# Kernel tuning notes

Measured on AMD Instinct MI355X. Metric: run time of the kernel, lower is better.

The kernel has to match this reference:

```python
import jax, jax.numpy as jnp
import numpy as np

B, T, QL, KVL, D, H = 4, 512, 2, 1, 1024, 16
N = T * QL          # query tokens for self-attn
HD = D // H
MLP_H = 4 * D
EPS_ADA = 1e-6
EPS_LN = 1e-5
NEG = -10000.0


def _ln(x, eps):
    mu = jnp.mean(x, axis=-1, keepdims=True)
    xc = x - mu
    var = jnp.mean(xc * xc, axis=-1, keepdims=True)
    return xc * jax.lax.rsqrt(var + eps)


def _attention(xq, xk, xv, wq, wk, wv, wo, bo, mask, pad_add):
    # xq:[B,Nq,D] xk/xv:[B,Nk,D]; mask:[Nq,Nk] bool; pad_add:[B,1,1,Nk]
    qh = (xq @ wq).reshape(B, -1, H, HD).transpose(0, 2, 1, 3)
    kh = (xk @ wk).reshape(B, -1, H, HD).transpose(0, 2, 1, 3)
    vh = (xv @ wv).reshape(B, -1, H, HD).transpose(0, 2, 1, 3)
    dots = jnp.einsum('bhnd,bhmd->bhnm', qh, kh) * (HD ** -0.5)
    dots = jnp.where(mask[None, None], dots, jnp.asarray(NEG, dots.dtype))
    dots = dots + pad_add
    attn = jax.nn.softmax(dots, axis=-1)
    out = jnp.einsum('bhnm,bhmd->bhnd', attn, vh)
    out = out.transpose(0, 2, 1, 3).reshape(B, -1, D)
    return out @ wo + bo


def setup_inputs() -> dict:
    key = jax.random.key(0)
    ks = jax.random.split(key, 32)
    s = 0.02
    d = {
        'q': jax.random.normal(ks[0], (B, N, D), jnp.float32),
        'c': jax.random.normal(ks[1], (B, T, D), jnp.float32),
        'pe': jax.random.normal(ks[2], (B, T, D), jnp.float32),
        'padding_mask': jax.random.randint(ks[3], (B, T), 0, 2, jnp.int32),
        'w_mod': jax.random.normal(ks[4], (D, 6 * D), jnp.float32) * s,
        'b_mod': jnp.zeros((6 * D,), jnp.float32),
        'sa_wq': jax.random.normal(ks[5], (D, D), jnp.float32) * s,
        'sa_wk': jax.random.normal(ks[6], (D, D), jnp.float32) * s,
        'sa_wv': jax.random.normal(ks[7], (D, D), jnp.float32) * s,
        'sa_wo': jax.random.normal(ks[8], (D, D), jnp.float32) * s,
        'sa_bo': jnp.zeros((D,), jnp.float32),
        'ca_wq': jax.random.normal(ks[9], (D, D), jnp.float32) * s,
        'ca_wk': jax.random.normal(ks[10], (D, D), jnp.float32) * s,
        'ca_wv': jax.random.normal(ks[11], (D, D), jnp.float32) * s,
        'ca_wo': jax.random.normal(ks[12], (D, D), jnp.float32) * s,
        'ca_bo': jnp.zeros((D,), jnp.float32),
        'gk': jnp.ones((D,), jnp.float32), 'bk': jnp.zeros((D,), jnp.float32),
        'gv': jnp.ones((D,), jnp.float32), 'bv': jnp.zeros((D,), jnp.float32),
        'w_alpha': jax.random.normal(ks[13], (2 * D, D), jnp.float32) * s,
        'b_alpha': jnp.zeros((D,), jnp.float32),
        'w1': jax.random.normal(ks[14], (D, MLP_H), jnp.float32) * s,
        'b1': jnp.zeros((MLP_H,), jnp.float32),
        'w2': jax.random.normal(ks[15], (MLP_H, D), jnp.float32) * s,
        'b2': jnp.zeros((D,), jnp.float32),
    }
    return d


def reference(q, c, pe, padding_mask, w_mod, b_mod,
              sa_wq, sa_wk, sa_wv, sa_wo, sa_bo,
              ca_wq, ca_wk, ca_wv, ca_wo, ca_bo,
              gk, bk, gv, bv, w_alpha, b_alpha, w1, b1, w2, b2):
    # AdaLN modulation from condition c
    mod = jax.nn.silu(c) @ w_mod + b_mod                    # [B,T,6D]
    scale_sa, shift_sa, scale_ca, shift_ca, scale_mlp, shift_mlp = jnp.split(mod, 6, axis=2)
    rep = lambda t: jnp.repeat(t, QL, axis=1)               # [B,T,D]->[B,N,D]

    # masks
    causal = jnp.tril(jnp.ones((N, N), bool))
    tril_t = jnp.tril(jnp.ones((T, T), bool))
    cross_mask = jnp.repeat(jnp.repeat(tril_t, QL, axis=0), KVL, axis=1)  # [N, T*KVL]
    pad_f = padding_mask.astype(q.dtype)
    pad_sa = (jnp.repeat(pad_f, QL, axis=1) * NEG)[:, None, None, :]      # keys len N
    pad_ca = (jnp.repeat(pad_f, KVL, axis=1) * NEG)[:, None, None, :]     # keys len T

    # self-attention (pre-norm + modulation)
    q1 = _ln(q, EPS_ADA) * (1 + rep(scale_sa)) + rep(shift_sa)
    q1 = _attention(q1, q1, q1, sa_wq, sa_wk, sa_wv, sa_wo, sa_bo, causal, pad_sa)
    q = q1 + q

    # cross-attention with custom mask
    q2 = _ln(q, EPS_ADA) * (1 + rep(scale_ca)) + rep(shift_ca)
    kin = _ln(c + pe, EPS_LN) * gk + bk
    vin = _ln(c, EPS_LN) * gv + bv
    q2 = _attention(q2, kin, vin, ca_wq, ca_wk, ca_wv, ca_wo, ca_bo, cross_mask, pad_ca)
    alpha = jnp.concatenate([q2, q], axis=-1) @ w_alpha + b_alpha
    q = (1 + alpha) * q2 + q

    # MLP
    q3 = _ln(q, EPS_ADA) * (1 + rep(scale_mlp)) + rep(shift_mlp)
    h = jax.nn.gelu(q3 @ w1 + b1, approximate=False)
    q = q + (h @ w2 + b2)
    return q
```

## Files before the change

### kernel.cpp

```cpp
#include <hip/hip_runtime.h>
#include <cstdint>

typedef unsigned short u16;
typedef __attribute__((ext_vector_type(8))) short bf16x8;
typedef __attribute__((ext_vector_type(4))) float f32x4;

#define DEV static __device__ __forceinline__
#define AS1 __attribute__((address_space(1)))
#define AS3 __attribute__((address_space(3)))

static constexpr int Bb = 4, Tt = 512, Nn = 1024, Dd = 1024, Hh = 16;
static constexpr float NEGV = -10000.0f;

DEV u16 f2bf(float f) {
  unsigned int u = __builtin_bit_cast(unsigned int, f);
  u += 0x7fffu + ((u >> 16) & 1u);
  return (u16)(u >> 16);
}
DEV float bf2f(u16 s) {
  unsigned int u = ((unsigned int)s) << 16;
  return __builtin_bit_cast(float, u);
}
DEV f32x4 mfma16(bf16x8 a, bf16x8 b, f32x4 c) {
  return __builtin_amdgcn_mfma_f32_16x16x32_bf16(a, b, c, 0, 0, 0);
}
DEV void gload16(const u16* g, u16* lds) {
  __builtin_amdgcn_global_load_lds((AS1 const unsigned int*)g, (AS3 unsigned int*)lds, 16, 0, 0);
}
DEV int swz8(int wg, int nwg) { const int c = nwg >> 3; return (wg & 7) * c + (wg >> 3); }

__global__ __launch_bounds__(256) void transpose_cast(const float* __restrict__ src,
                                                      u16* __restrict__ dst, int R, int C) {
  __shared__ float tile[32][33];
  const int c0 = blockIdx.x * 32, r0 = blockIdx.y * 32;
  const int tx = threadIdx.x, ty = threadIdx.y;
#pragma unroll
  for (int j = 0; j < 4; ++j)
    tile[ty + 8 * j][tx] = src[(size_t)(r0 + ty + 8 * j) * C + c0 + tx];
  __syncthreads();
#pragma unroll
  for (int j = 0; j < 4; ++j)
    dst[(size_t)(c0 + ty + 8 * j) * R + r0 + tx] = f2bf(tile[tx][ty + 8 * j]);
}

__global__ __launch_bounds__(256) void tr16_k(const u16* __restrict__ src, u16* __restrict__ dst,
                                              int ss, int R) {
  __shared__ u16 tile[32][33];
  const int c0 = blockIdx.x * 32, r0 = blockIdx.y * 32;
  const int tx = threadIdx.x, ty = threadIdx.y;
#pragma unroll
  for (int j = 0; j < 4; ++j)
    tile[ty + 8 * j][tx] = src[(size_t)(r0 + ty + 8 * j) * ss + c0 + tx];
  __syncthreads();
  const int b = r0 / R, rb = r0 - b * R;
#pragma unroll
  for (int j = 0; j < 4; ++j)
    dst[(size_t)b * 1024 * R + (size_t)(c0 + ty + 8 * j) * R + rb + tx] = tile[tx][ty + 8 * j];
}

__global__ __launch_bounds__(256) void silu_k(const float* __restrict__ c, u16* __restrict__ o, int n) {
  int i = blockIdx.x * 256 + threadIdx.x;
  if (i < n) { float x = c[i]; o[i] = f2bf(x / (1.0f + __expf(-x))); }
}

__global__ __launch_bounds__(256) void cat_k(const float* __restrict__ q2, const float* __restrict__ qr,
                                             u16* __restrict__ cat) {
  int i = blockIdx.x * 256 + threadIdx.x;
  int r = i >> 10, c = i & 1023;
  cat[(size_t)r * 2048 + c] = f2bf(q2[i]);
  cat[(size_t)r * 2048 + 1024 + c] = f2bf(qr[i]);
}

__global__ __launch_bounds__(256) void red2_k(const u16* __restrict__ s0, const u16* __restrict__ s1,
                                              const float* __restrict__ bias, const float* __restrict__ res,
                                              float* __restrict__ out) {
  const int i = blockIdx.x * 256 + threadIdx.x;
  const uint2 a = ((const uint2*)s0)[i];
  const uint2 b = ((const uint2*)s1)[i];
  const float4 bv = ((const float4*)bias)[i & 255];
  const float4 rv = ((const float4*)res)[i];
  float4 v;
  v.x = bf2f((u16)(a.x & 0xffff)) + bf2f((u16)(b.x & 0xffff)) + bv.x + rv.x;
  v.y = bf2f((u16)(a.x >> 16))    + bf2f((u16)(b.x >> 16))    + bv.y + rv.y;
  v.z = bf2f((u16)(a.y & 0xffff)) + bf2f((u16)(b.y & 0xffff)) + bv.z + rv.z;
  v.w = bf2f((u16)(a.y >> 16))    + bf2f((u16)(b.y >> 16))    + bv.w + rv.w;
  ((float4*)out)[i] = v;
}

__global__ __launch_bounds__(64) void mrow_k(const int* __restrict__ pm, float* __restrict__ M) {
  const int tid = threadIdx.x;
  const int b = tid >> 4, seg = tid & 15;
  int pre[32];
  int a = 1;
#pragma unroll
  for (int j = 0; j < 32; ++j) { a &= pm[b * 512 + seg * 32 + j]; pre[j] = a; }
  const int total = a;
  int excl = 1;
  for (int s = 0; s < 16; ++s) {
    int o = __shfl(total, (b << 4) + s, 64);
    if (s < seg) excl &= o;
  }
#pragma unroll
  for (int j = 0; j < 32; ++j)
    M[b * 512 + seg * 32 + j] = (excl & pre[j]) ? NEGV : 0.0f;
}

__global__ __launch_bounds__(256) void ln_mod_k(const float* __restrict__ X, const u16* __restrict__ MOD,
                                                u16* __restrict__ OUT, int chunk) {
  const int row = blockIdx.x;
  const int b = row >> 10, i = row & 1023, t = i >> 1;
  const int tid = threadIdx.x;
  const float4 xv = *(const float4*)&X[(size_t)row * 1024 + tid * 4];
  float s = xv.x + xv.y + xv.z + xv.w;
  float q = xv.x * xv.x + xv.y * xv.y + xv.z * xv.z + xv.w * xv.w;
#pragma unroll
  for (int off = 32; off > 0; off >>= 1) { s += __shfl_down(s, off); q += __shfl_down(q, off); }
  __shared__ float rs[4], rq[4];
  if ((tid & 63) == 0) { rs[tid >> 6] = s; rq[tid >> 6] = q; }
  __syncthreads();
  float S = rs[0] + rs[1] + rs[2] + rs[3];
  float Q = rq[0] + rq[1] + rq[2] + rq[3];
  const float mu = S * (1.0f / 1024.0f);
  const float var = Q * (1.0f / 1024.0f) - mu * mu;
  const float rstd = rsqrtf(var + 1e-6f);
  const u16* mrow = MOD + (size_t)(b * Tt + t) * 6144 + chunk * 1024 + tid * 4;
  u16* out = OUT + (size_t)row * 1024 + tid * 4;
  const float xx[4] = {xv.x, xv.y, xv.z, xv.w};
#pragma unroll
  for (int j = 0; j < 4; ++j) {
    float sc = bf2f(mrow[j]);
    float sh = bf2f(mrow[1024 + j]);
    out[j] = f2bf((xx[j] - mu) * rstd * (1.0f + sc) + sh);
  }
}

__global__ __launch_bounds__(256) void ln_kv_k(const float* __restrict__ C_, const float* __restrict__ PE,
                                               const float* __restrict__ gk, const float* __restrict__ bk,
                                               const float* __restrict__ gv, const float* __restrict__ bv,
                                               u16* __restrict__ KIN, u16* __restrict__ VIN) {
  const int row = blockIdx.x, tid = threadIdx.x;
  const size_t base = (size_t)row * 1024 + tid * 4;
  const float4 cv = *(const float4*)&C_[base];
  const float4 pv = *(const float4*)&PE[base];
  const float a[4] = {cv.x + pv.x, cv.y + pv.y, cv.z + pv.z, cv.w + pv.w};
  const float bb[4] = {cv.x, cv.y, cv.z, cv.w};
  float sa = a[0] + a[1] + a[2] + a[3];
  float qa = a[0] * a[0] + a[1] * a[1] + a[2] * a[2] + a[3] * a[3];
  float sb = bb[0] + bb[1] + bb[2] + bb[3];
  float qb = bb[0] * bb[0] + bb[1] * bb[1] + bb[2] * bb[2] + bb[3] * bb[3];
#pragma unroll
  for (int off = 32; off > 0; off >>= 1) {
    sa += __shfl_down(sa, off); qa += __shfl_down(qa, off);
    sb += __shfl_down(sb, off); qb += __shfl_down(qb, off);
  }
  __shared__ float r4[4][4];
  if ((tid & 63) == 0) {
    int w = tid >> 6;
    r4[0][w] = sa; r4[1][w] = qa; r4[2][w] = sb; r4[3][w] = qb;
  }
  __syncthreads();
  sa = r4[0][0] + r4[0][1] + r4[0][2] + r4[0][3];
  qa = r4[1][0] + r4[1][1] + r4[1][2] + r4[1][3];
  sb = r4[2][0] + r4[2][1] + r4[2][2] + r4[2][3];
  qb = r4[3][0] + r4[3][1] + r4[3][2] + r4[3][3];
  const float mua = sa * (1.0f / 1024.0f);
  const float ra = rsqrtf(qa * (1.0f / 1024.0f) - mua * mua + 1e-5f);
  const float mub = sb * (1.0f / 1024.0f);
  const float rb = rsqrtf(qb * (1.0f / 1024.0f) - mub * mub + 1e-5f);
#pragma unroll
  for (int j = 0; j < 4; ++j) {
    int d = tid * 4 + j;
    KIN[(size_t)row * 1024 + d] = f2bf((a[j] - mua) * ra * gk[d] + bk[d]);
    VIN[(size_t)row * 1024 + d] = f2bf((bb[j] - mub) * rb * gv[d] + bv[d]);
  }
}

DEV void stage32(const u16* __restrict__ A, const u16* __restrict__ Bt, int K,
                 int brow, int bcol, int kb, u16 (*As)[32], u16 (*Bs)[32]) {
  const int l = threadIdx.x & 63, wid = threadIdx.x >> 6;
#pragma unroll
  for (int p = 0; p < 2; ++p) {
    const int r0 = p * 64 + wid * 16;
    const int row = r0 + (l >> 2), kof = (l & 3) << 3;
    gload16(&A[(size_t)(brow + row) * K + kb + kof], &As[r0][0]);
    gload16(&Bt[(size_t)(bcol + row) * K + kb + kof], &Bs[r0][0]);
  }
}

DEV void gcore(const u16* __restrict__ A, const u16* __restrict__ Bt, int K,
               int brow, int bcol, int k0, int nk32,
               u16 (*As)[128][32], u16 (*Bs)[128][32], f32x4 (&acc)[4][4]) {
  const int l = threadIdx.x & 63, wid = threadIdx.x >> 6;
  const int wr = wid >> 1, wc = wid & 1;
  const int fr = l & 15, fg = l >> 4;
  stage32(A, Bt, K, brow, bcol, k0, As[0], Bs[0]);
  __syncthreads();
  int cur = 0;
  for (int kt = 0; kt < nk32; ++kt) {
    if (kt + 1 < nk32)
      stage32(A, Bt, K, brow, bcol, k0 + ((kt + 1) << 5), As[cur ^ 1], Bs[cur ^ 1]);
    bf16x8 af[4], bfr[4];
#pragma unroll
    for (int m = 0; m < 4; ++m) af[m] = *(const bf16x8*)&As[cur][wr * 64 + m * 16 + fr][fg * 8];
#pragma unroll
    for (int n = 0; n < 4; ++n) bfr[n] = *(const bf16x8*)&Bs[cur][wc * 64 + n * 16 + fr][fg * 8];
#pragma unroll
    for (int m = 0; m < 4; ++m)
#pragma unroll
      for (int n = 0; n < 4; ++n) acc[m][n] = mfma16(af[m], bfr[n], acc[m][n]);
    __syncthreads();
    cur ^= 1;
  }
}

template <int EPI>
__global__ __launch_bounds__(256) void gemm_k(const u16* __restrict__ A, const u16* __restrict__ Bt,
                                              int N, int K, const float* __restrict__ bias,
                                              u16* __restrict__ outb, int nbx) {
  __shared__ u16 As[2][128][32];
  __shared__ u16 Bs[2][128][32];
  const int wg = swz8(blockIdx.x, gridDim.x);
  const int brow = (wg / nbx) * 128, bcol = (wg % nbx) * 128;
  const int l = threadIdx.x & 63, wid = threadIdx.x >> 6;
  const int wr = wid >> 1, wc = wid & 1, fr = l & 15, fg = l >> 4;
  f32x4 acc[4][4];
#pragma unroll
  for (int m = 0; m < 4; ++m)
#pragma unroll
    for (int n = 0; n < 4; ++n) acc[m][n] = (f32x4){0.f, 0.f, 0.f, 0.f};
  gcore(A, Bt, K, brow, bcol, 0, K >> 5, As, Bs, acc);
#pragma unroll
  for (int m = 0; m < 4; ++m)
#pragma unroll
    for (int n = 0; n < 4; ++n)
#pragma unroll
      for (int r = 0; r < 4; ++r) {
        const int row = brow + wr * 64 + m * 16 + fg * 4 + r;
        const int col = bcol + wc * 64 + n * 16 + fr;
        float v = acc[m][n][r];
        if (EPI != 0) v += bias[col];
        if (EPI == 2) {
          const float u = v * (0.7978845608f + 0.0356774081f * v * v);
          v = v / (1.0f + __expf(-2.0f * u));
        }
        outb[(size_t)row * N + col] = f2bf(v);
      }
}

template <int EPI>
__global__ __launch_bounds__(256) void gemm64(const u16* __restrict__ A, const u16* __restrict__ Bt,
                                              int N, int K, const float* __restrict__ bias,
                                              const float* __restrict__ res, const float* __restrict__ q2,
                                              float* __restrict__ outf, int nbx) {
  __shared__ u16 As[2][128][32];
  __shared__ u16 Bs[2][64][32];
  const int wg = swz8(blockIdx.x, gridDim.x);
  const int brow = (wg / nbx) * 128, bcol = (wg % nbx) * 64;
  const int l = threadIdx.x & 63, wid = threadIdx.x >> 6;
  const int wr = wid >> 1, wc = wid & 1, fr = l & 15, fg = l >> 4;
  const int srow = l >> 2, skof = (l & 3) << 3;

  f32x4 acc[4][2];
#pragma unroll
  for (int m = 0; m < 4; ++m)
#pragma unroll
    for (int n = 0; n < 2; ++n) acc[m][n] = (f32x4){0.f, 0.f, 0.f, 0.f};

  auto stg = [&](int kb, int cur) {
    gload16(&A[(size_t)(brow + wid * 32 + srow) * K + kb + skof], &As[cur][wid * 32][0]);
    gload16(&A[(size_t)(brow + wid * 32 + 16 + srow) * K + kb + skof], &As[cur][wid * 32 + 16][0]);
    gload16(&Bt[(size_t)(bcol + wid * 16 + srow) * K + kb + skof], &Bs[cur][wid * 16][0]);
  };

  stg(0, 0);
  __syncthreads();
  int cur = 0;
  const int nk32 = K >> 5;
  for (int kt = 0; kt < nk32; ++kt) {
    if (kt + 1 < nk32) stg((kt + 1) << 5, cur ^ 1);
    bf16x8 af[4], bfr[2];
#pragma unroll
    for (int m = 0; m < 4; ++m) af[m] = *(const bf16x8*)&As[cur][wr * 64 + m * 16 + fr][fg * 8];
#pragma unroll
    for (int n = 0; n < 2; ++n) bfr[n] = *(const bf16x8*)&Bs[cur][wc * 32 + n * 16 + fr][fg * 8];
#pragma unroll
    for (int m = 0; m < 4; ++m)
#pragma unroll
      for (int n = 0; n < 2; ++n) acc[m][n] = mfma16(af[m], bfr[n], acc[m][n]);
    __syncthreads();
    cur ^= 1;
  }

#pragma unroll
  for (int m = 0; m < 4; ++m)
#pragma unroll
    for (int n = 0; n < 2; ++n)
#pragma unroll
      for (int r = 0; r < 4; ++r) {
        const int row = brow + wr * 64 + m * 16 + fg * 4 + r;
        const int col = bcol + wc * 32 + n * 16 + fr;
        const size_t o = (size_t)row * N + col;
        const float v = acc[m][n][r] + bias[col];
        if (EPI == 3) outf[o] = v + res[o];
        else if (EPI == 4) outf[o] = v;
        else outf[o] = (1.0f + v) * q2[o] + outf[o];
      }
}

__global__ __launch_bounds__(256) void gemm64b(const u16* __restrict__ A, const u16* __restrict__ Bt,
                                               int N, int K, u16* __restrict__ sk0, u16* __restrict__ sk1,
                                               int nbx) {
  __shared__ u16 As[2][128][32];
  __shared__ u16 Bs[2][64][32];
  const int wg = swz8(blockIdx.x, gridDim.x);
  const int brow = (wg / nbx) * 128, bcol = (wg % nbx) * 64;
  const int kper = K >> 1;
  const int k0 = blockIdx.y * kper;
  const int l = threadIdx.x & 63, wid = threadIdx.x >> 6;
  const int wr = wid >> 1, wc = wid & 1, fr = l & 15, fg = l >> 4;
  const int srow = l >> 2, skof = (l & 3) << 3;

  f32x4 acc[4][2];
#pragma unroll
  for (int m = 0; m < 4; ++m)
#pragma unroll
    for (int n = 0; n < 2; ++n) acc[m][n] = (f32x4){0.f, 0.f, 0.f, 0.f};

  auto stg = [&](int kb, int cur) {
    gload16(&A[(size_t)(brow + wid * 32 + srow) * K + kb + skof], &As[cur][wid * 32][0]);
    gload16(&A[(size_t)(brow + wid * 32 + 16 + srow) * K + kb + skof], &As[cur][wid * 32 + 16][0]);
    gload16(&Bt[(size_t)(bcol + wid * 16 + srow) * K + kb + skof], &Bs[cur][wid * 16][0]);
  };

  stg(k0, 0);
  __syncthreads();
  int cur = 0;
  const int nk32 = kper >> 5;
  for (int kt = 0; kt < nk32; ++kt) {
    if (kt + 1 < nk32) stg(k0 + ((kt + 1) << 5), cur ^ 1);
    bf16x8 af[4], bfr[2];
#pragma unroll
    for (int m = 0; m < 4; ++m) af[m] = *(const bf16x8*)&As[cur][wr * 64 + m * 16 + fr][fg * 8];
#pragma unroll
    for (int n = 0; n < 2; ++n) bfr[n] = *(const bf16x8*)&Bs[cur][wc * 32 + n * 16 + fr][fg * 8];
#pragma unroll
    for (int m = 0; m < 4; ++m)
#pragma unroll
      for (int n = 0; n < 2; ++n) acc[m][n] = mfma16(af[m], bfr[n], acc[m][n]);
    __syncthreads();
    cur ^= 1;
  }

  u16* out = blockIdx.y ? sk1 : sk0;
#pragma unroll
  for (int m = 0; m < 4; ++m)
#pragma unroll
    for (int n = 0; n < 2; ++n)
#pragma unroll
      for (int r = 0; r < 4; ++r) {
        const int row = brow + wr * 64 + m * 16 + fg * 4 + r;
        const int col = bcol + wc * 32 + n * 16 + fr;
        out[(size_t)row * N + col] = f2bf(acc[m][n][r]);
      }
}

__global__ __launch_bounds__(256) void gemm3_k(const u16* A0, const u16* A1, const u16* A2,
                                               const u16* B0, const u16* B1, const u16* B2,
                                               u16* O0, u16* O1, u16* O2) {
  const int z = blockIdx.y;
  const int wg = swz8(blockIdx.x, gridDim.x);
  const int bx = wg & 7, by = wg >> 3;
  if (z > 0 && by >= 16) return;
  const u16* A = z == 0 ? A0 : (z == 1 ? A1 : A2);
  const u16* Bt = z == 0 ? B0 : (z == 1 ? B1 : B2);
  u16* O = z == 0 ? O0 : (z == 1 ? O1 : O2);
  __shared__ u16 As[2][128][32];
  __shared__ u16 Bs[2][128][32];
  const int brow = by * 128, bcol = bx * 128;
  const int l = threadIdx.x & 63, wid = threadIdx.x >> 6;
  const int wr = wid >> 1, wc = wid & 1, fr = l & 15, fg = l >> 4;
  f32x4 acc[4][4];
#pragma unroll
  for (int m = 0; m < 4; ++m)
#pragma unroll
    for (int n = 0; n < 4; ++n) acc[m][n] = (f32x4){0.f, 0.f, 0.f, 0.f};
  gcore(A, Bt, 1024, brow, bcol, 0, 32, As, Bs, acc);
#pragma unroll
  for (int m = 0; m < 4; ++m)
#pragma unroll
    for (int n = 0; n < 4; ++n)
#pragma unroll
      for (int r = 0; r < 4; ++r) {
        const int row = brow + wr * 64 + m * 16 + fg * 4 + r;
        const int col = bcol + wc * 64 + n * 16 + fr;
        O[(size_t)row * 1024 + col] = f2bf(acc[m][n][r]);
      }
}

template <int QDIV, int PDIV>
__global__ __launch_bounds__(256) void attn_k(const u16* __restrict__ QH, const u16* __restrict__ KH,
                                              const u16* __restrict__ VT, u16* __restrict__ AO,
                                              const int* __restrict__ pmask, const float* __restrict__ Mrow,
                                              int Nq, int Nk, int qs, int ks) {
  __shared__ u16 KS[2][2048];
  __shared__ u16 VS[2][2048];
  __shared__ u16 PL[4][16][40];
  const int tid = threadIdx.x;
  const int l = tid & 63, wid = tid >> 6;
  const int fr = l & 15, fg = l >> 4;
  const int nqb = Nq >> 6;
  const int wgid = swz8(blockIdx.x, gridDim.x);
  const int qb = wgid % nqb;
  const int bh = wgid / nqb;
  const int h = bh & 15, b = bh >> 4;
  const int q0 = qb * 64 + wid * 16;

  u16 (*Pl)[40] = PL[wid];

  const int krow = l >> 3;
  const int kslot = (l & 7) ^ krow;
  const int vrow = l >> 2;
  const int vslot = (l & 3) ^ (vrow & 3);

  const size_t qrow = (size_t)(b * Nq + q0 + fr) * qs + h * 64;
  const bf16x8 aq0 = *(const bf16x8*)&QH[qrow + fg * 8];
  const bf16x8 aq1 = *(const bf16x8*)&QH[qrow + 32 + fg * 8];

  float Mr[4];
#pragma unroll
  for (int r = 0; r < 4; ++r) Mr[r] = Mrow[b * Tt + ((q0 + fg * 4 + r) >> 1)];

  f32x4 o[4];
#pragma unroll
  for (int c = 0; c < 4; ++c) o[c] = (f32x4){0.f, 0.f, 0.f, 0.f};
  float lsum[4] = {0.f, 0.f, 0.f, 0.f};

  int nkt = Nk >> 5;
  if (Mrow[b * Tt + ((qb * 64) >> 1)] == 0.0f) {
    const int kallow = (qb * 64 + 63) / QDIV + 1;
    const int t = (kallow + 31) >> 5;
    if (t < nkt) nkt = t;
  }

  const int sw0 = (fg ^ (fr & 7)) * 8;
  const int sw1 = ((4 + fg) ^ (fr & 7)) * 8;
  const size_t vtb = (size_t)b * 1024 * Nk + (size_t)(h * 64) * Nk;

  auto stage = [&](int kb, int buf) {
    gload16(&KH[(size_t)(b * Nk + kb + wid * 8 + krow) * ks + h * 64 + kslot * 8], &KS[buf][wid * 512]);
    gload16(&VT[vtb + (size_t)(wid * 16 + vrow) * Nk + kb + vslot * 8], &VS[buf][wid * 512]);
  };

  stage(0, 0);
  __syncthreads();
  int buf = 0;

  for (int kt = 0; kt < nkt; ++kt) {
    const int kb = kt << 5;
    if (kt + 1 < nkt) stage((kt + 1) << 5, buf ^ 1);

    const u16* Ksl = KS[buf];
    const u16* Vsl = VS[buf];

    f32x4 s0 = (f32x4){0.f, 0.f, 0.f, 0.f}, s1 = (f32x4){0.f, 0.f, 0.f, 0.f};
    {
      bf16x8 kf;
      kf = *(const bf16x8*)&Ksl[fr * 64 + sw0];        s0 = mfma16(aq0, kf, s0);
      kf = *(const bf16x8*)&Ksl[fr * 64 + sw1];        s0 = mfma16(aq1, kf, s0);
      kf = *(const bf16x8*)&Ksl[(16 + fr) * 64 + sw0]; s1 = mfma16(aq0, kf, s1);
      kf = *(const bf16x8*)&Ksl[(16 + fr) * 64 + sw1]; s1 = mfma16(aq1, kf, s1);
    }
    const int c0 = kb + fr, c1 = kb + 16 + fr;
    const float pad0 = pmask[b * Tt + (PDIV == 2 ? (c0 >> 1) : c0)] ? NEGV : 0.0f;
    const float pad1 = pmask[b * Tt + (PDIV == 2 ? (c1 >> 1) : c1)] ? NEGV : 0.0f;

#pragma unroll
    for (int r = 0; r < 4; ++r) {
      const int rq = (q0 + fg * 4 + r) >> (QDIV == 2 ? 1 : 0);
      float v0 = s0[r] * 0.125f; v0 = (c0 <= rq) ? v0 : NEGV; v0 += pad0;
      float v1 = s1[r] * 0.125f; v1 = (c1 <= rq) ? v1 : NEGV; v1 += pad1;
      const float p0 = __expf(v0 - Mr[r]);
      const float p1 = __expf(v1 - Mr[r]);
      lsum[r] += p0 + p1;
      Pl[fg * 4 + r][fr] = f2bf(p0);
      Pl[fg * 4 + r][16 + fr] = f2bf(p1);
    }

    const bf16x8 pa = *(const bf16x8*)&Pl[fr][fg * 8];
#pragma unroll
    for (int c = 0; c < 4; ++c) {
      const bf16x8 vb = *(const bf16x8*)&Vsl[(c * 16 + fr) * 32 + ((fg ^ (fr & 3)) << 3)];
      o[c] = mfma16(pa, vb, o[c]);
    }
    __syncthreads();
    buf ^= 1;
  }

#pragma unroll
  for (int r = 0; r < 4; ++r) {
    lsum[r] += __shfl_xor(lsum[r], 1);
    lsum[r] += __shfl_xor(lsum[r], 2);
    lsum[r] += __shfl_xor(lsum[r], 4);
    lsum[r] += __shfl_xor(lsum[r], 8);
  }

#pragma unroll
  for (int c = 0; c < 4; ++c)
#pragma unroll
    for (int r = 0; r < 4; ++r) {
      const int row = q0 + fg * 4 + r;
      AO[(size_t)(b * Nq + row) * Dd + h * 64 + c * 16 + fr] = f2bf(o[c][r] / lsum[r]);
    }
}

extern "C" void kernel_launch(void* const* d_in, const int* in_sizes, int n_in,
                              void* d_out, int out_size, void* d_ws, size_t ws_size,
                              hipStream_t stream) {
  (void)in_sizes; (void)n_in; (void)out_size; (void)ws_size;
  const float* q_in   = (const float*)d_in[0];
  const float* c_in   = (const float*)d_in[1];
  const float* pe     = (const float*)d_in[2];
  const int*   pmask  = (const int*)d_in[3];
  const float* w_mod  = (const float*)d_in[4];
  const float* b_mod  = (const float*)d_in[5];
  const float* sa_wq  = (const float*)d_in[6];
  const float* sa_wk  = (const float*)d_in[7];
  const float* sa_wv  = (const float*)d_in[8];
  const float* sa_wo  = (const float*)d_in[9];
  const float* sa_bo  = (const float*)d_in[10];
  const float* ca_wq  = (const float*)d_in[11];
  const float* ca_wk  = (const float*)d_in[12];
  const float* ca_wv  = (const float*)d_in[13];
  const float* ca_wo  = (const float*)d_in[14];
  const float* ca_bo  = (const float*)d_in[15];
  const float* gk     = (const float*)d_in[16];
  const float* bk     = (const float*)d_in[17];
  const float* gv     = (const float*)d_in[18];
  const float* bv     = (const float*)d_in[19];
  const float* w_alpha= (const float*)d_in[20];
  const float* b_alpha= (const float*)d_in[21];
  const float* w1     = (const float*)d_in[22];
  const float* b1     = (const float*)d_in[23];
  const float* w2     = (const float*)d_in[24];
  const float* b2     = (const float*)d_in[25];

  u16* ws = (u16*)d_ws;
  u16* WMODt  = ws + 0;
  float* Mp   = (float*)(ws + 4194304);
  u16* SK1b   = WMODt;
  u16* SAWQt  = ws + 6291456;
  u16* SAWKt  = ws + 7340032;
  u16* SAWVt  = ws + 8388608;
  u16* SAWOt  = ws + 9437184;
  u16* CAWQt  = ws + 10485760;
  u16* CAWKt  = ws + 11534336;
  u16* CAWVt  = ws + 12582912;
  u16* CAWOt  = ws + 13631488;
  u16* WALPHt = ws + 14680064;
  u16* W1t    = ws + 16777216;
  u16* W2t    = ws + 20971520;
  u16* Xs     = ws + 25165824;
  u16* KINp   = Xs;
  u16* VINp   = SAWQt;
  u16* MODbf  = ws + 27262976;
  u16* LNO    = ws + 39845888;
  u16* SK0b   = LNO;
  u16* BIG    = ws + 44040192;
  u16* QKVp = BIG;
  u16* VTsa = BIG + 12582912;
  u16* AOp  = LNO;
  u16* CAQp = BIG;
  u16* CAKp = BIG + 4194304;
  u16* CAVp = BIG + 6291456;
  u16* VT2  = BIG + 8388608;
  u16* AO2p = BIG + 10485760;
  u16* CATp = BIG;
  u16* HBp  = BIG;
  float* Qres = (float*)(ws + 60817408);
  float* Q2f  = Qres + 4194304;
  float* outp = (float*)d_out;

  const dim3 blk(256);
  auto TR = [&](const float* s, u16* d, int R, int C) {
    transpose_cast<<<dim3(C / 32, R / 32), dim3(32, 8), 0, stream>>>(s, d, R, C);
  };

  TR(w_mod, WMODt, 1024, 6144);
  TR(sa_wq, SAWQt, 1024, 1024); TR(sa_wk, SAWKt, 1024, 1024);
  TR(sa_wv, SAWVt, 1024, 1024); TR(sa_wo, SAWOt, 1024, 1024);
  TR(ca_wq, CAWQt, 1024, 1024); TR(ca_wk, CAWKt, 1024, 1024);
  TR(ca_wv, CAWVt, 1024, 1024); TR(ca_wo, CAWOt, 1024, 1024);
  TR(w_alpha, WALPHt, 2048, 1024);
  TR(w1, W1t, 1024, 4096);
  TR(w2, W2t, 4096, 1024);

  silu_k<<<8192, blk, 0, stream>>>(c_in, Xs, 2048 * 1024);
  gemm_k<1><<<768, blk, 0, stream>>>(Xs, WMODt, 6144, 1024, b_mod, MODbf, 48);
  mrow_k<<<1, 64, 0, stream>>>(pmask, Mp);

  ln_mod_k<<<4096, blk, 0, stream>>>(q_in, MODbf, LNO, 0);
  gemm_k<0><<<768, blk, 0, stream>>>(LNO, SAWQt, 3072, 1024, nullptr, QKVp, 24);
  tr16_k<<<dim3(32, 128), dim3(32, 8), 0, stream>>>(QKVp + 2048, VTsa, 3072, 1024);
  ln_kv_k<<<2048, blk, 0, stream>>>(c_in, pe, gk, bk, gv, bv, KINp, VINp);
  attn_k<1, 2><<<1024, blk, 0, stream>>>(QKVp, QKVp + 1024, VTsa, AOp, pmask, Mp,
                                         1024, 1024, 3072, 3072);
  gemm64<3><<<512, blk, 0, stream>>>(AOp, SAWOt, 1024, 1024, sa_bo, q_in, nullptr, Qres, 16);

  ln_mod_k<<<4096, blk, 0, stream>>>(Qres, MODbf, LNO, 2);
  gemm3_k<<<dim3(256, 3), blk, 0, stream>>>(LNO, KINp, VINp, CAWQt, CAWKt, CAWVt, CAQp, CAKp, CAVp);
  tr16_k<<<dim3(32, 64), dim3(32, 8), 0, stream>>>(CAVp, VT2, 1024, 512);
  attn_k<2, 1><<<1024, blk, 0, stream>>>(CAQp, CAKp, VT2, AO2p, pmask, Mp,
                                         1024, 512, 1024, 1024);
  gemm64<4><<<512, blk, 0, stream>>>(AO2p, CAWOt, 1024, 1024, ca_bo, nullptr, nullptr, Q2f, 16);
  cat_k<<<16384, blk, 0, stream>>>(Q2f, Qres, CATp);
  gemm64<5><<<512, blk, 0, stream>>>(CATp, WALPHt, 1024, 2048, b_alpha, nullptr, Q2f, Qres, 16);

  ln_mod_k<<<4096, blk, 0, stream>>>(Qres, MODbf, LNO, 4);
  gemm_k<2><<<1024, blk, 0, stream>>>(LNO, W1t, 4096, 1024, b1, HBp, 32);
  gemm64b<<<dim3(512, 2), blk, 0, stream>>>(HBp, W2t, 1024, 4096, SK0b, SK1b, 16);
  red2_k<<<4096, blk, 0, stream>>>(SK0b, SK1b, b2, Qres, outp);
}
```

Measured before the change: 480.5 us.

## Replace full syncthreads with split lgkm/vmcnt barriers and cache pad mask in LDS

Each double-buffered GEMM and attention loop now uses two barriers: one waits on LDS reads before reusing a buffer, the other waits with a partial vmcnt so the next tile's global-to-LDS prefetch can stay in flight while the current tile is computed. The attention kernel also stages the padding mask as additive floats in shared memory once per block instead of reloading from global every key tile. This trims stall time at barriers and redundant global loads, but relies on hand-written waitcnt counts matching the number of issued loads, which could silently break correctness if the count is wrong.

```diff
diff --git a/kernel.cpp b/kernel.cpp
--- a/kernel.cpp
+++ b/kernel.cpp
@@ -28,6 +28,18 @@
   __builtin_amdgcn_global_load_lds((AS1 const unsigned int*)g, (AS3 unsigned int*)lds, 16, 0, 0);
 }
 DEV int swz8(int wg, int nwg) { const int c = nwg >> 3; return (wg & 7) * c + (wg >> 3); }
+
+DEV void bar_lgkm0() {
+  asm volatile("s_waitcnt lgkmcnt(0)" ::: "memory");
+  __builtin_amdgcn_s_barrier();
+  __builtin_amdgcn_sched_barrier(0);
+}
+#define BAR_VM(N)                                          \
+  do {                                                     \
+    asm volatile("s_waitcnt vmcnt(" #N ")" ::: "memory");  \
+    __builtin_amdgcn_s_barrier();                          \
+    __builtin_amdgcn_sched_barrier(0);                     \
+  } while (0)
 
 __global__ __launch_bounds__(256) void transpose_cast(const float* __restrict__ src,
                                                       u16* __restrict__ dst, int R, int C) {
@@ -194,11 +206,15 @@
   const int wr = wid >> 1, wc = wid & 1;
   const int fr = l & 15, fg = l >> 4;
   stage32(A, Bt, K, brow, bcol, k0, As[0], Bs[0]);
-  __syncthreads();
   int cur = 0;
   for (int kt = 0; kt < nk32; ++kt) {
-    if (kt + 1 < nk32)
+    bar_lgkm0();
+    if (kt + 1 < nk32) {
       stage32(A, Bt, K, brow, bcol, k0 + ((kt + 1) << 5), As[cur ^ 1], Bs[cur ^ 1]);
+      BAR_VM(4);
+    } else {
+      BAR_VM(0);
+    }
     bf16x8 af[4], bfr[4];
 #pragma unroll
     for (int m = 0; m < 4; ++m) af[m] = *(const bf16x8*)&As[cur][wr * 64 + m * 16 + fr][fg * 8];
@@ -208,9 +224,9 @@
     for (int m = 0; m < 4; ++m)
 #pragma unroll
       for (int n = 0; n < 4; ++n) acc[m][n] = mfma16(af[m], bfr[n], acc[m][n]);
-    __syncthreads();
     cur ^= 1;
   }
+  __syncthreads();
 }
 
 template <int EPI>
@@ -273,11 +289,16 @@
   };
 
   stg(0, 0);
-  __syncthreads();
   int cur = 0;
   const int nk32 = K >> 5;
   for (int kt = 0; kt < nk32; ++kt) {
-    if (kt + 1 < nk32) stg((kt + 1) << 5, cur ^ 1);
+    bar_lgkm0();
+    if (kt + 1 < nk32) {
+      stg((kt + 1) << 5, cur ^ 1);
+      BAR_VM(3);
+    } else {
+      BAR_VM(0);
+    }
     bf16x8 af[4], bfr[2];
 #pragma unroll
     for (int m = 0; m < 4; ++m) af[m] = *(const bf16x8*)&As[cur][wr * 64 + m * 16 + fr][fg * 8];
@@ -287,7 +308,6 @@
     for (int m = 0; m < 4; ++m)
 #pragma unroll
       for (int n = 0; n < 2; ++n) acc[m][n] = mfma16(af[m], bfr[n], acc[m][n]);
-    __syncthreads();
     cur ^= 1;
   }
 
@@ -333,11 +353,16 @@
   };
 
   stg(k0, 0);
-  __syncthreads();
   int cur = 0;
   const int nk32 = kper >> 5;
   for (int kt = 0; kt < nk32; ++kt) {
-    if (kt + 1 < nk32) stg(k0 + ((kt + 1) << 5), cur ^ 1);
+    bar_lgkm0();
+    if (kt + 1 < nk32) {
+      stg(k0 + ((kt + 1) << 5), cur ^ 1);
+      BAR_VM(3);
+    } else {
+      BAR_VM(0);
+    }
     bf16x8 af[4], bfr[2];
 #pragma unroll
     for (int m = 0; m < 4; ++m) af[m] = *(const bf16x8*)&As[cur][wr * 64 + m * 16 + fr][fg * 8];
@@ -347,7 +372,6 @@
     for (int m = 0; m < 4; ++m)
 #pragma unroll
       for (int n = 0; n < 2; ++n) acc[m][n] = mfma16(af[m], bfr[n], acc[m][n]);
-    __syncthreads();
     cur ^= 1;
   }
 
@@ -405,6 +429,7 @@
   __shared__ u16 KS[2][2048];
   __shared__ u16 VS[2][2048];
   __shared__ u16 PL[4][16][40];
+  __shared__ float Padd[512];
   const int tid = threadIdx.x;
   const int l = tid & 63, wid = tid >> 6;
   const int fr = l & 15, fg = l >> 4;
@@ -422,6 +447,9 @@
   const int vrow = l >> 2;
   const int vslot = (l & 3) ^ (vrow & 3);
 
+  Padd[tid] = pmask[b * Tt + tid] ? NEGV : 0.0f;
+  Padd[256 + tid] = pmask[b * Tt + 256 + tid] ? NEGV : 0.0f;
+
   const size_t qrow = (size_t)(b * Nq + q0 + fr) * qs + h * 64;
   const bf16x8 aq0 = *(const bf16x8*)&QH[qrow + fg * 8];
   const bf16x8 aq1 = *(const bf16x8*)&QH[qrow + 32 + fg * 8];
@@ -451,13 +479,19 @@
     gload16(&VT[vtb + (size_t)(wid * 16 + vrow) * Nk + kb + vslot * 8], &VS[buf][wid * 512]);
   };
 
+  __syncthreads();
   stage(0, 0);
-  __syncthreads();
   int buf = 0;
 
   for (int kt = 0; kt < nkt; ++kt) {
     const int kb = kt << 5;
-    if (kt + 1 < nkt) stage((kt + 1) << 5, buf ^ 1);
+    bar_lgkm0();
+    if (kt + 1 < nkt) {
+      stage((kt + 1) << 5, buf ^ 1);
+      BAR_VM(2);
+    } else {
+      BAR_VM(0);
+    }
 
     const u16* Ksl = KS[buf];
     const u16* Vsl = VS[buf];
@@ -471,8 +505,8 @@
       kf = *(const bf16x8*)&Ksl[(16 + fr) * 64 + sw1]; s1 = mfma16(aq1, kf, s1);
     }
     const int c0 = kb + fr, c1 = kb + 16 + fr;
-    const float pad0 = pmask[b * Tt + (PDIV == 2 ? (c0 >> 1) : c0)] ? NEGV : 0.0f;
-    const float pad1 = pmask[b * Tt + (PDIV == 2 ? (c1 >> 1) : c1)] ? NEGV : 0.0f;
+    const float pad0 = Padd[PDIV == 2 ? (c0 >> 1) : c0];
+    const float pad1 = Padd[PDIV == 2 ? (c1 >> 1) : c1];
 
 #pragma unroll
     for (int r = 0; r < 4; ++r) {
@@ -492,7 +526,6 @@
       const bf16x8 vb = *(const bf16x8*)&Vsl[(c * 16 + fr) * 32 + ((fg ^ (fr & 3)) << 3)];
       o[c] = mfma16(pa, vb, o[c]);
     }
-    __syncthreads();
     buf ^= 1;
   }
 
```

Measured after the change: 483.4 us. No clear change (+0.6%).
